# Kernel optimization log

Measured on AMD Instinct MI355X. Metric: run time of the kernel, lower is better.

The kernel has to match this reference:

```python
import jax, jax.numpy as jnp
import numpy as np

N_NODES = 100000
N_EDGES = 1000000
IN_FEATS = 128
HID_FEATS = 128
OUT_FEATS = 128
N_CLASSES = 16
NEG_SLOPE = 0.01
BN_EPS = 1e-5


def _linear_params(key, d_in, d_out):
    k1, k2 = jax.random.split(key)
    s = 1.0 / np.sqrt(d_in)
    w = jax.random.uniform(k1, (d_in, d_out), jnp.float32, -s, s)
    b = jax.random.uniform(k2, (d_out,), jnp.float32, -s, s)
    return w, b


def setup_inputs() -> dict:
    key = jax.random.key(0)
    ks = jax.random.split(key, 16)
    node_feat = jax.random.normal(ks[0], (N_NODES, IN_FEATS), jnp.float32)
    src = jax.random.randint(ks[1], (N_EDGES,), 0, N_NODES, jnp.int32)
    dst = jax.random.randint(ks[2], (N_EDGES,), 0, N_NODES, jnp.int32)
    dims = [(IN_FEATS, HID_FEATS), (HID_FEATS, HID_FEATS), (HID_FEATS, OUT_FEATS)]
    inp = {"node_feat": node_feat, "src": src, "dst": dst}
    for i, (din, dout) in enumerate(dims):
        wp, bp = _linear_params(ks[3 + 4 * i], din, din)      # fc_pool: d_in -> d_in
        ws, _ = _linear_params(ks[4 + 4 * i], din, dout)       # fc_self (no bias)
        wn, _ = _linear_params(ks[5 + 4 * i], din, dout)       # fc_neigh (no bias)
        _, b = _linear_params(ks[6 + 4 * i], din, dout)        # shared output bias
        inp[f"wp{i}"] = wp; inp[f"bp{i}"] = bp
        inp[f"ws{i}"] = ws; inp[f"wn{i}"] = wn; inp[f"b{i}"] = b
    inp["bn_gamma"] = jnp.ones((HID_FEATS,), jnp.float32)
    inp["bn_beta"] = jnp.zeros((HID_FEATS,), jnp.float32)
    wc, bc = _linear_params(ks[15], OUT_FEATS, N_CLASSES)
    inp["wc"] = wc; inp["bc"] = bc
    return inp


def _sage_pool(h, src, dst, deg_mask, wp, bp, ws, wn, b):
    # fc_pool + relu on source nodes, gather per edge, segment-max to dst
    hp = jax.nn.relu(h @ wp + bp)                 # [N, d_in]
    msg = hp[src]                                 # [E, d_in]
    agg = jax.ops.segment_max(msg, dst, num_segments=N_NODES)  # [N, d_in]
    agg = jnp.where(deg_mask, agg, 0.0)           # zero for isolated nodes
    return h @ ws + agg @ wn + b


def _batchnorm(x, gamma, beta):
    mu = jnp.mean(x, axis=0)
    var = jnp.var(x, axis=0)
    return (x - mu) * jax.lax.rsqrt(var + BN_EPS) * gamma + beta


def reference(node_feat, src, dst,
              wp0, bp0, ws0, wn0, b0,
              wp1, bp1, ws1, wn1, b1,
              wp2, bp2, ws2, wn2, b2,
              bn_gamma, bn_beta, wc, bc):
    deg = jnp.zeros((N_NODES,), jnp.float32).at[dst].add(1.0)
    deg_mask = (deg > 0)[:, None]
    h = jax.nn.leaky_relu(_sage_pool(node_feat, src, dst, deg_mask, wp0, bp0, ws0, wn0, b0), NEG_SLOPE)
    h = jax.nn.leaky_relu(_batchnorm(_sage_pool(h, src, dst, deg_mask, wp1, bp1, ws1, wn1, b1), bn_gamma, bn_beta), NEG_SLOPE)
    h = _sage_pool(h, src, dst, deg_mask, wp2, bp2, ws2, wn2, b2)
    return h @ wc + bc
```

## Files before the change

kernel.cpp:

```cpp
#include <hip/hip_runtime.h>


#define N_NODES 100000
#define N_EDGES 1000000
#define F 128
#define NEG_SLOPE 0.01f
#define BN_EPS 1e-5f
#define NODES_PER_XCD 12500

typedef __attribute__((ext_vector_type(8))) short bf16x8;
typedef __attribute__((ext_vector_type(4))) float f32x4;
typedef __attribute__((ext_vector_type(2))) unsigned short u16x2;

typedef __attribute__((address_space(3))) unsigned int as3_uint;
typedef __attribute__((address_space(1))) const unsigned int as1_cuint;

__device__ __forceinline__ void gload16(const void* g, void* l) {
    __builtin_amdgcn_global_load_lds((as1_cuint*)g, (as3_uint*)l, 16, 0, 0);
}

__device__ __forceinline__ unsigned short f2bf(float f) {
    unsigned int u = __float_as_uint(f);
    u += 0x7fff + ((u >> 16) & 1);
    return (unsigned short)(u >> 16);
}
__device__ __forceinline__ float bf2f(unsigned short h) {
    return __uint_as_float(((unsigned int)h) << 16);
}

__global__ __launch_bounds__(256) void zero_kernel(float4* __restrict__ p, long n4) {
    long i = (long)blockIdx.x * 256 + threadIdx.x;
    if (i < n4) p[i] = make_float4(0.f, 0.f, 0.f, 0.f);
}

__global__ __launch_bounds__(256) void f32_to_bf16_kernel(
    const float4* __restrict__ in, uint2* __restrict__ out, long n4)
{
    long i = (long)blockIdx.x * 256 + threadIdx.x;
    if (i >= n4) return;
    float4 v = in[i];
    uint2 o;
    o.x = (unsigned)f2bf(v.x) | ((unsigned)f2bf(v.y) << 16);
    o.y = (unsigned)f2bf(v.z) | ((unsigned)f2bf(v.w) << 16);
    out[i] = o;
}

__global__ __launch_bounds__(256) void pack_weights3(
    const float* __restrict__ wp, const float* __restrict__ wss,
    const float* __restrict__ wn, short* __restrict__ wp_p, short* __restrict__ wsn_p)
{
    const int i = blockIdx.x * 256 + threadIdx.x;
    if (i >= 3 * 16384) return;
    const int mat = i >> 14;
    const int idx = i & 16383;
    const int k = idx >> 7, n = idx & 127;
    const float* srcm = mat == 0 ? wp : (mat == 1 ? wss : wn);
    const int slot = ((k >> 3) * 128 + n) * 8 + (k & 7);
    if (mat == 0) wp_p[slot] = (short)f2bf(srcm[idx]);
    else wsn_p[(mat == 2 ? 16 * 128 * 8 : 0) + slot] = (short)f2bf(srcm[idx]);
}

template<int NKS>
__global__ __launch_bounds__(256) void gemm_mfma(
    const short* __restrict__ A1, const short* __restrict__ A2,
    const short* __restrict__ Bp, const float* __restrict__ bias,
    unsigned short* __restrict__ Cout, int n_rows, int act)
{
    constexpr int S = NKS / 2;
    __shared__ short tile[2 * 8192];

    const int tid = threadIdx.x;
    const int wave = tid >> 6;
    const int lane = tid & 63;
    const int m = lane & 15, q = lane >> 4;
    const int r0 = blockIdx.x * 128;
    const int rw = (wave >> 1) * 64;
    const int r0q = r0 + rw;
    const int c0 = (wave & 1) * 64;
    const int gchunk = (tid & 7) ^ ((tid >> 3) & 7);

    f32x4 acc[4][4];
#pragma unroll
    for (int i = 0; i < 4; ++i)
#pragma unroll
        for (int j = 0; j < 4; ++j)
#pragma unroll
            for (int r = 0; r < 4; ++r) acc[i][j][r] = 0.f;

    auto stage = [&](int s, int buf) {
        const short* Ap = (NKS == 8 && s >= 2) ? A2 : A1;
        const int kbase = (s & 1) * 64;
#pragma unroll
        for (int p = 0; p < 4; ++p) {
            int row = r0 + (tid >> 3) + 32 * p;
            row = min(row, n_rows - 1);
            gload16(Ap + (size_t)row * F + kbase + gchunk * 8,
                    &tile[buf * 8192 + p * 2048 + tid * 8]);
        }
    };

    stage(0, 0);
    __syncthreads();

    for (int s = 0; s < S; ++s) {
        if (s + 1 < S) stage(s + 1, (s + 1) & 1);
        const short* tb = &tile[(s & 1) * 8192];
#pragma unroll
        for (int ks2 = 0; ks2 < 2; ++ks2) {
            const int ks32 = s * 2 + ks2;
            bf16x8 b[4], a[4];
#pragma unroll
            for (int ni = 0; ni < 4; ++ni)
                b[ni] = *(const bf16x8*)(Bp + ((size_t)(ks32 * 4 + q) * F + c0 + ni * 16 + m) * 8);
#pragma unroll
            for (int mi = 0; mi < 4; ++mi)
                a[mi] = *(const bf16x8*)(tb + (rw + mi * 16 + m) * 64 + (((ks2 * 4 + q) ^ (m & 7)) << 3));
#pragma unroll
            for (int mi = 0; mi < 4; ++mi)
#pragma unroll
                for (int ni = 0; ni < 4; ++ni)
                    acc[mi][ni] = __builtin_amdgcn_mfma_f32_16x16x32_bf16(a[mi], b[ni], acc[mi][ni], 0, 0, 0);
        }
        __syncthreads();
    }

    float bv[4];
#pragma unroll
    for (int ni = 0; ni < 4; ++ni) bv[ni] = bias[c0 + ni * 16 + m];

    short* ep = &tile[wave * 1280];
    const int colc_lo = m >> 3, cin = m & 7;
#pragma unroll
    for (int mi = 0; mi < 4; ++mi) {
#pragma unroll
        for (int ni = 0; ni < 4; ++ni) {
            const int colc = 2 * ni + colc_lo;
#pragma unroll
            for (int rg = 0; rg < 4; ++rg) {
                const int row16 = q * 4 + rg;
                float v = acc[mi][ni][rg] + bv[ni];
                if (act == 1) v = v > 0.f ? v : 0.f;
                else if (act == 2) v = v > 0.f ? v : v * NEG_SLOPE;
                ep[row16 * 80 + ((colc ^ (row16 & 7)) << 3) + cin] = (short)f2bf(v);
            }
        }
        __syncthreads();
#pragma unroll
        for (int p = 0; p < 2; ++p) {
            const int lrow = (lane >> 3) + 8 * p;
            bf16x8 vv = *(const bf16x8*)&ep[lrow * 80 + (((lane & 7) ^ (lrow & 7)) << 3)];
            const int grow = r0q + mi * 16 + lrow;
            if (grow < n_rows)
                *(bf16x8*)(Cout + (size_t)grow * F + c0 + ((lane & 7) << 3)) = vv;
        }
        __syncthreads();
    }
}

__global__ __launch_bounds__(256) void hist_kernel(const int* __restrict__ dst, int* __restrict__ deg) {
    const int e = blockIdx.x * 256 + threadIdx.x;
    if (e < N_EDGES) atomicAdd(&deg[__builtin_nontemporal_load(&dst[e])], 1);
}

__global__ __launch_bounds__(256) void scan1_kernel(const int* __restrict__ deg, int* __restrict__ bsum) {
    __shared__ int sh[256];
    const int t = threadIdx.x;
    const int base = blockIdx.x * 1024 + t * 4;
    int s = 0;
#pragma unroll
    for (int j = 0; j < 4; ++j) s += (base + j < N_NODES) ? deg[base + j] : 0;
    sh[t] = s; __syncthreads();
    for (int off = 128; off; off >>= 1) {
        if (t < off) sh[t] += sh[t + off];
        __syncthreads();
    }
    if (t == 0) bsum[blockIdx.x] = sh[0];
}

__global__ __launch_bounds__(128) void scan2_kernel(int* __restrict__ bsum, int nb, int* __restrict__ row_start) {
    __shared__ int sh[128];
    const int t = threadIdx.x;
    sh[t] = (t < nb) ? bsum[t] : 0;
    __syncthreads();
    for (int off = 1; off < 128; off <<= 1) {
        int x = (t >= off) ? sh[t - off] : 0;
        __syncthreads();
        if (t >= off) sh[t] += x;
        __syncthreads();
    }
    if (t < nb) bsum[t] = t ? sh[t - 1] : 0;
    if (t == 0) row_start[N_NODES] = N_EDGES;
}

__global__ __launch_bounds__(256) void scan3_kernel(
    const int* __restrict__ deg, const int* __restrict__ boff,
    int* __restrict__ row_start, int* __restrict__ cursor)
{
    __shared__ int sh[256];
    const int t = threadIdx.x;
    const int base = blockIdx.x * 1024 + t * 4;
    int v[4]; int s = 0;
#pragma unroll
    for (int j = 0; j < 4; ++j) { v[j] = (base + j < N_NODES) ? deg[base + j] : 0; s += v[j]; }
    sh[t] = s; __syncthreads();
    for (int off = 1; off < 256; off <<= 1) {
        int x = (t >= off) ? sh[t - off] : 0;
        __syncthreads();
        if (t >= off) sh[t] += x;
        __syncthreads();
    }
    int excl = (t ? sh[t - 1] : 0) + boff[blockIdx.x];
#pragma unroll
    for (int j = 0; j < 4; ++j) {
        if (base + j < N_NODES) { row_start[base + j] = excl; cursor[base + j] = excl; }
        excl += v[j];
    }
}

#define CHUNK_E2 1954
__global__ __launch_bounds__(256) void scatter_xcd_kernel(
    const int* __restrict__ src, const int* __restrict__ dst,
    int* __restrict__ cursor, int* __restrict__ esrc)
{
    const int range = blockIdx.x & 7;
    const int chunk = blockIdx.x >> 3;
    const int lo = range * NODES_PER_XCD;
    const int e0 = chunk * CHUNK_E2;
    const int e1 = min(e0 + CHUNK_E2, N_EDGES);
    for (int e = e0 + threadIdx.x; e < e1; e += 256) {
        const int d = dst[e];
        if ((unsigned)(d - lo) < NODES_PER_XCD) {
            const int pos = atomicAdd(&cursor[d], 1);
            esrc[pos] = src[e];
        }
    }
}

__global__ __launch_bounds__(256) void aggregate_max_bf16(
    const unsigned int* __restrict__ hp, const int* __restrict__ row_start,
    const int* __restrict__ esrc, unsigned int* __restrict__ agg)
{
    const int node = blockIdx.x * 4 + (threadIdx.x >> 6);
    if (node >= N_NODES) return;
    const int lane = threadIdx.x & 63;
    const int beg = row_start[node], end = row_start[node + 1];
    u16x2 mm = (u16x2)0;
    for (int base = beg; base < end; base += 16) {
        int s[16];
#pragma unroll
        for (int j = 0; j < 16; ++j) {
            const int t = base + j;
            s[j] = esrc[(t < end) ? t : beg];
        }
        unsigned int v[16];
#pragma unroll
        for (int j = 0; j < 16; ++j) v[j] = hp[(size_t)s[j] * 64 + lane];
#pragma unroll
        for (int j = 0; j < 16; ++j)
            mm = __builtin_elementwise_max(mm, __builtin_bit_cast(u16x2, v[j]));
    }
    agg[(size_t)node * 64 + lane] = __builtin_bit_cast(unsigned int, mm);
}

#define BN_ROWS_PER_BLOCK 196
__global__ __launch_bounds__(256) void bn_stats_kernel(
    const unsigned short* __restrict__ x, float* __restrict__ stats, int n)
{
    const int tid = threadIdx.x;
    const int wave = tid >> 6, lane = tid & 63;
    const int rgrp = lane >> 4;
    const int c16 = lane & 15;
    const int rbase = blockIdx.x * BN_ROWS_PER_BLOCK;
    const int rend = min(rbase + BN_ROWS_PER_BLOCK, n);

    float s[8], ss[8];
#pragma unroll
    for (int j = 0; j < 8; ++j) { s[j] = 0.f; ss[j] = 0.f; }

    for (int r = rbase + wave * 4 + rgrp; r < rend; r += 16) {
        const uint4 v = *(const uint4*)(x + (size_t)r * F + c16 * 8);
        const unsigned int w[4] = {v.x, v.y, v.z, v.w};
#pragma unroll
        for (int u = 0; u < 4; ++u) {
            const float f0 = bf2f((unsigned short)(w[u] & 0xffffu));
            const float f1 = bf2f((unsigned short)(w[u] >> 16));
            s[2*u]   += f0; ss[2*u]   = fmaf(f0, f0, ss[2*u]);
            s[2*u+1] += f1; ss[2*u+1] = fmaf(f1, f1, ss[2*u+1]);
        }
    }
#pragma unroll
    for (int j = 0; j < 8; ++j) {
        s[j]  += __shfl_down(s[j], 32);  s[j]  += __shfl_down(s[j], 16);
        ss[j] += __shfl_down(ss[j], 32); ss[j] += __shfl_down(ss[j], 16);
    }
    __shared__ float sh[4][16][16];
    if (lane < 16) {
#pragma unroll
        for (int j = 0; j < 8; ++j) {
            sh[wave][c16][2*j]     = s[j];
            sh[wave][c16][2*j + 1] = ss[j];
        }
    }
    __syncthreads();
    const float tot = sh[0][tid >> 4][tid & 15] + sh[1][tid >> 4][tid & 15]
                    + sh[2][tid >> 4][tid & 15] + sh[3][tid >> 4][tid & 15];
    const int col = (tid >> 4) * 8 + ((tid >> 1) & 7);
    atomicAdd(&stats[(tid & 1) * 128 + col], tot);
}

__global__ void bn_finalize_kernel(
    const float* __restrict__ stats, const float* __restrict__ gamma,
    const float* __restrict__ beta, float* __restrict__ coef)
{
    const int c = threadIdx.x;
    const float mean = stats[c] * (1.f / N_NODES);
    const float var = stats[128 + c] * (1.f / N_NODES) - mean * mean;
    const float scale = gamma[c] * rsqrtf(var + BN_EPS);
    coef[c] = scale;
    coef[128 + c] = fmaf(-mean, scale, beta[c]);
}

__global__ __launch_bounds__(256) void bn_apply_bf16(
    unsigned int* __restrict__ x, const float* __restrict__ coef, long n2)
{
    __shared__ float sc[128], sf[128];
    if (threadIdx.x < 128) {
        sc[threadIdx.x] = coef[threadIdx.x];
        sf[threadIdx.x] = coef[128 + threadIdx.x];
    }
    __syncthreads();
    const long i = (long)blockIdx.x * 256 + threadIdx.x;
    if (i >= n2) return;
    const unsigned int v = x[i];
    const int c0 = (int)(i & 63) * 2;
    float a = fmaf(bf2f((unsigned short)(v & 0xffffu)), sc[c0], sf[c0]);
    float b = fmaf(bf2f((unsigned short)(v >> 16)), sc[c0 + 1], sf[c0 + 1]);
    a = a > 0.f ? a : a * NEG_SLOPE;
    b = b > 0.f ? b : b * NEG_SLOPE;
    x[i] = (unsigned)f2bf(a) | ((unsigned)f2bf(b) << 16);
}

__global__ __launch_bounds__(256) void classifier_kernel(
    const unsigned short* __restrict__ X, const float* __restrict__ Wc,
    const float* __restrict__ bc, float* __restrict__ out, int n)
{
    __shared__ float Wl[2048];
    __shared__ float Xs[16 * 132];
    const int tid = threadIdx.x;
    for (int i = tid; i < 2048; i += 256) Wl[i] = Wc[i];
    const int r0 = blockIdx.x * 16;
    for (int i = tid; i < 2048; i += 256) {
        const int row = i >> 7, col = i & 127;
        const int gr = r0 + row;
        Xs[row * 132 + col] = (gr < n) ? bf2f(X[(size_t)gr * F + col]) : 0.f;
    }
    __syncthreads();
    const int rl = tid >> 4, c = tid & 15;
    const int r = r0 + rl;
    if (r >= n) return;
    float s = bc[c];
    const float* xr = &Xs[rl * 132];
#pragma unroll
    for (int k = 0; k < 128; ++k) s = fmaf(xr[k], Wl[k * 16 + c], s);
    out[(size_t)r * 16 + c] = s;
}

extern "C" void kernel_launch(void* const* d_in, const int* in_sizes, int n_in,
                              void* d_out, int out_size, void* d_ws, size_t ws_size,
                              hipStream_t stream) {
    const float* node_feat = (const float*)d_in[0];
    const int* src = (const int*)d_in[1];
    const int* dst = (const int*)d_in[2];
    const float* wp[3] = {(const float*)d_in[3],  (const float*)d_in[8],  (const float*)d_in[13]};
    const float* bp[3] = {(const float*)d_in[4],  (const float*)d_in[9],  (const float*)d_in[14]};
    const float* wsm[3] = {(const float*)d_in[5], (const float*)d_in[10], (const float*)d_in[15]};
    const float* wn[3] = {(const float*)d_in[6],  (const float*)d_in[11], (const float*)d_in[16]};
    const float* bb[3] = {(const float*)d_in[7],  (const float*)d_in[12], (const float*)d_in[17]};
    const float* gamma = (const float*)d_in[18];
    const float* beta  = (const float*)d_in[19];
    const float* wc    = (const float*)d_in[20];
    const float* bc    = (const float*)d_in[21];

    const size_t SZ = (size_t)N_NODES * F;
    short* sbase = (short*)d_ws;
    short* B0  = sbase;
    short* B1  = sbase + SZ;
    short* B2  = sbase + 2 * SZ;
    short* Xbf = sbase + 3 * SZ;
    short* wp_p  = sbase + 4 * SZ;
    short* wsn_p = wp_p + 3 * 16384;
    float* fbase = (float*)(wsn_p + 3 * 32768);
    float* stats = fbase;
    float* coef  = fbase + 256;
    int* ibase = (int*)(fbase + 512);
    int* deg       = ibase;
    int* row_start = ibase + 100000;
    int* cursor    = ibase + 200104;
    int* esrc      = ibase + 300104;
    int* bsum      = ibase + 1300104;

    const int gGemm = (N_NODES + 127) / 128;
    const int gE    = (N_EDGES + 255) / 256;
    const int gScan = (N_NODES + 1023) / 1024;
    const int gAgg  = (N_NODES + 3) / 4;
    const long cvt4 = (long)(SZ / 4);
    const long n2   = (long)(SZ / 2);

    f32_to_bf16_kernel<<<(int)((cvt4 + 255) / 256), 256, 0, stream>>>(
        (const float4*)node_feat, (uint2*)Xbf, cvt4);
    for (int l = 0; l < 3; ++l)
        pack_weights3<<<192, 256, 0, stream>>>(wp[l], wsm[l], wn[l],
                                               wp_p + l * 16384, wsn_p + l * 32768);

    zero_kernel<<<98, 256, 0, stream>>>((float4*)deg, 25000);
    hist_kernel<<<gE, 256, 0, stream>>>(dst, deg);
    scan1_kernel<<<gScan, 256, 0, stream>>>(deg, bsum);
    scan2_kernel<<<1, 128, 0, stream>>>(bsum, gScan, row_start);
    scan3_kernel<<<gScan, 256, 0, stream>>>(deg, bsum, row_start, cursor);
    scatter_xcd_kernel<<<4096, 256, 0, stream>>>(src, dst, cursor, esrc);

    const short* Xl[3]  = {Xbf, B0, B1};
    short* hpb[3]       = {B0, B1, B0};
    short* aggb[3]      = {B1, B2, B2};
    short* Yb[3]        = {B0, B1, B0};
    for (int l = 0; l < 3; ++l) {
        const short* X = Xl[l];
        gemm_mfma<4><<<gGemm, 256, 0, stream>>>(X, (const short*)nullptr,
            wp_p + l * 16384, bp[l], (unsigned short*)hpb[l], N_NODES, 1);
        aggregate_max_bf16<<<gAgg, 256, 0, stream>>>(
            (const unsigned int*)hpb[l], row_start, esrc, (unsigned int*)aggb[l]);
        const int act = (l == 0) ? 2 : 0;
        gemm_mfma<8><<<gGemm, 256, 0, stream>>>(X, aggb[l],
            wsn_p + l * 32768, bb[l], (unsigned short*)Yb[l], N_NODES, act);
        if (l == 1) {
            zero_kernel<<<1, 256, 0, stream>>>((float4*)stats, 64);
            bn_stats_kernel<<<512, 256, 0, stream>>>(
                (const unsigned short*)Yb[l], stats, N_NODES);
            bn_finalize_kernel<<<1, 128, 0, stream>>>(stats, gamma, beta, coef);
            bn_apply_bf16<<<(int)((n2 + 255) / 256), 256, 0, stream>>>(
                (unsigned int*)Yb[l], coef, n2);
        }
    }
    classifier_kernel<<<(N_NODES + 15) / 16, 256, 0, stream>>>(
        (const unsigned short*)B0, wc, bc, (float*)d_out, N_NODES);
}
```

Measured before the change: 554.6 us.

## Fuse prep kernels and overlap edge scatter with layer-0 pool GEMM

Three pieces of setup work are merged into one launch each. The feature conversion, degree histogram and weight packing now run as one prep kernel, and the two zeroing launches become one. The CSR edge scatter and the first fc_pool GEMM now share a single kernel with interleaved block roles, so the GEMM can fill the machine while the scatter is bound by atomics. The scatter also loads 16 edges per thread with batched atomics. This removes several launches and their gaps, at the cost of heterogeneous blocks competing for resources such as LDS and registers in the fused kernel.

Measured after the change: 529.2 us. 1.05x faster.

```diff
diff --git a/kernel.cpp b/kernel.cpp
--- a/kernel.cpp
+++ b/kernel.cpp
@@ -28,43 +28,71 @@
     return __uint_as_float(((unsigned int)h) << 16);
 }
 
-__global__ __launch_bounds__(256) void zero_kernel(float4* __restrict__ p, long n4) {
-    long i = (long)blockIdx.x * 256 + threadIdx.x;
-    if (i < n4) p[i] = make_float4(0.f, 0.f, 0.f, 0.f);
-}
-
-__global__ __launch_bounds__(256) void f32_to_bf16_kernel(
-    const float4* __restrict__ in, uint2* __restrict__ out, long n4)
-{
-    long i = (long)blockIdx.x * 256 + threadIdx.x;
-    if (i >= n4) return;
-    float4 v = in[i];
-    uint2 o;
-    o.x = (unsigned)f2bf(v.x) | ((unsigned)f2bf(v.y) << 16);
-    o.y = (unsigned)f2bf(v.z) | ((unsigned)f2bf(v.w) << 16);
-    out[i] = o;
-}
-
-__global__ __launch_bounds__(256) void pack_weights3(
-    const float* __restrict__ wp, const float* __restrict__ wss,
-    const float* __restrict__ wn, short* __restrict__ wp_p, short* __restrict__ wsn_p)
-{
-    const int i = blockIdx.x * 256 + threadIdx.x;
-    if (i >= 3 * 16384) return;
-    const int mat = i >> 14;
-    const int idx = i & 16383;
-    const int k = idx >> 7, n = idx & 127;
-    const float* srcm = mat == 0 ? wp : (mat == 1 ? wss : wn);
-    const int slot = ((k >> 3) * 128 + n) * 8 + (k & 7);
-    if (mat == 0) wp_p[slot] = (short)f2bf(srcm[idx]);
-    else wsn_p[(mat == 2 ? 16 * 128 * 8 : 0) + slot] = (short)f2bf(srcm[idx]);
+__global__ __launch_bounds__(256) void zero_misc_kernel(
+    float4* __restrict__ deg4, float4* __restrict__ stats4)
+{
+    if (blockIdx.x < 98) {
+        const int i = blockIdx.x * 256 + threadIdx.x;
+        if (i < 25000) deg4[i] = make_float4(0.f, 0.f, 0.f, 0.f);
+    } else {
+        if (threadIdx.x < 64) stats4[threadIdx.x] = make_float4(0.f, 0.f, 0.f, 0.f);
+    }
+}
+
+#define PREP_GROUPS 4483
+__global__ __launch_bounds__(256) void prep_kernel(
+    const float4* __restrict__ nf, uint2* __restrict__ xout,
+    const int* __restrict__ dst, int* __restrict__ deg,
+    const float* __restrict__ w0, const float* __restrict__ w1, const float* __restrict__ w2,
+    const float* __restrict__ w3, const float* __restrict__ w4, const float* __restrict__ w5,
+    const float* __restrict__ w6, const float* __restrict__ w7, const float* __restrict__ w8,
+    short* __restrict__ wp_p, short* __restrict__ wsn_p)
+{
+    const int g = blockIdx.x >> 2;
+    const int k = blockIdx.x & 3;
+    const int tid = threadIdx.x;
+    if (k < 3) {
+        const int c = g * 3 + k;
+        if (c >= 12500) return;
+        const long i = (long)c * 256 + tid;
+        float4 v = nf[i];
+        uint2 o;
+        o.x = (unsigned)f2bf(v.x) | ((unsigned)f2bf(v.y) << 16);
+        o.y = (unsigned)f2bf(v.z) | ((unsigned)f2bf(v.w) << 16);
+        xout[i] = o;
+        return;
+    }
+    if (g < 3907) {
+        const int e = g * 256 + tid;
+        if (e < N_EDGES) atomicAdd(&deg[__builtin_nontemporal_load(&dst[e])], 1);
+        return;
+    }
+    const int po = g - 3907;
+    if (po >= 576) return;
+    const int idx = po * 256 + tid;
+    const int matid = idx >> 14;
+    const int layer = (matid * 11) >> 5;
+    const int mat = matid - 3 * layer;
+    const int i = idx & 16383;
+    const int kk = i >> 7, n = i & 127;
+    const float* srcm;
+    switch (matid) {
+        case 0: srcm = w0; break; case 1: srcm = w1; break; case 2: srcm = w2; break;
+        case 3: srcm = w3; break; case 4: srcm = w4; break; case 5: srcm = w5; break;
+        case 6: srcm = w6; break; case 7: srcm = w7; break; default: srcm = w8; break;
+    }
+    const int slot = ((kk >> 3) * 128 + n) * 8 + (kk & 7);
+    const short v = (short)f2bf(srcm[i]);
+    if (mat == 0) wp_p[layer * 16384 + slot] = v;
+    else wsn_p[layer * 32768 + (mat == 2 ? 16384 : 0) + slot] = v;
 }
 
 template<int NKS>
-__global__ __launch_bounds__(256) void gemm_mfma(
+__device__ __forceinline__ void gemm_body(
+    const int bid,
     const short* __restrict__ A1, const short* __restrict__ A2,
     const short* __restrict__ Bp, const float* __restrict__ bias,
-    unsigned short* __restrict__ Cout, int n_rows, int act)
+    unsigned short* __restrict__ Cout, const int n_rows, const int act)
 {
     constexpr int S = NKS / 2;
     __shared__ short tile[2 * 8192];
@@ -73,7 +101,7 @@
     const int wave = tid >> 6;
     const int lane = tid & 63;
     const int m = lane & 15, q = lane >> 4;
-    const int r0 = blockIdx.x * 128;
+    const int r0 = bid * 128;
     const int rw = (wave >> 1) * 64;
     const int r0q = r0 + rw;
     const int c0 = (wave & 1) * 64;
@@ -157,9 +185,13 @@
     }
 }
 
-__global__ __launch_bounds__(256) void hist_kernel(const int* __restrict__ dst, int* __restrict__ deg) {
-    const int e = blockIdx.x * 256 + threadIdx.x;
-    if (e < N_EDGES) atomicAdd(&deg[__builtin_nontemporal_load(&dst[e])], 1);
+template<int NKS>
+__global__ __launch_bounds__(256) void gemm_mfma(
+    const short* __restrict__ A1, const short* __restrict__ A2,
+    const short* __restrict__ Bp, const float* __restrict__ bias,
+    unsigned short* __restrict__ Cout, int n_rows, int act)
+{
+    gemm_body<NKS>(blockIdx.x, A1, A2, Bp, bias, Cout, n_rows, act);
 }
 
 __global__ __launch_bounds__(256) void scan1_kernel(const int* __restrict__ deg, int* __restrict__ bsum) {
@@ -217,22 +249,45 @@
     }
 }
 
-#define CHUNK_E2 1954
-__global__ __launch_bounds__(256) void scatter_xcd_kernel(
+__global__ __launch_bounds__(256) void scatter_gemm_kernel(
     const int* __restrict__ src, const int* __restrict__ dst,
-    int* __restrict__ cursor, int* __restrict__ esrc)
-{
-    const int range = blockIdx.x & 7;
-    const int chunk = blockIdx.x >> 3;
-    const int lo = range * NODES_PER_XCD;
-    const int e0 = chunk * CHUNK_E2;
-    const int e1 = min(e0 + CHUNK_E2, N_EDGES);
-    for (int e = e0 + threadIdx.x; e < e1; e += 256) {
-        const int d = dst[e];
-        if ((unsigned)(d - lo) < NODES_PER_XCD) {
-            const int pos = atomicAdd(&cursor[d], 1);
-            esrc[pos] = src[e];
-        }
+    int* __restrict__ cursor, int* __restrict__ esrc,
+    const short* __restrict__ A1, const short* __restrict__ Bp,
+    const float* __restrict__ bias, unsigned short* __restrict__ Cout)
+{
+    const int bid = blockIdx.x;
+    const int grp = bid >> 3;
+    const int t8 = bid & 7;
+    const int sgrp = grp / 7;
+    const int u = grp - sgrp * 7;
+    if (u < 5) {
+        const int lo = t8 * NODES_PER_XCD;
+        const int chunk = sgrp * 5 + u;
+        const int e0 = chunk * 4096 + threadIdx.x;
+        int d[16]; bool hit[16];
+#pragma unroll
+        for (int j = 0; j < 16; ++j) {
+            const int e = e0 + j * 256;
+            d[j] = dst[min(e, N_EDGES - 1)];
+        }
+#pragma unroll
+        for (int j = 0; j < 16; ++j)
+            hit[j] = (e0 + j * 256 < N_EDGES) & ((unsigned)(d[j] - lo) < (unsigned)NODES_PER_XCD);
+        int sv[16];
+#pragma unroll
+        for (int j = 0; j < 16; ++j)
+            if (hit[j]) sv[j] = src[e0 + j * 256];
+        int pos[16];
+#pragma unroll
+        for (int j = 0; j < 16; ++j)
+            if (hit[j]) pos[j] = atomicAdd(&cursor[d[j]], 1);
+#pragma unroll
+        for (int j = 0; j < 16; ++j)
+            if (hit[j]) esrc[pos[j]] = sv[j];
+    } else {
+        const int g = (sgrp * 2 + (u - 5)) * 8 + t8;
+        if (g >= (N_NODES + 127) / 128) return;
+        gemm_body<4>(g, A1, (const short*)nullptr, Bp, bias, Cout, N_NODES, 1);
     }
 }
 
@@ -400,24 +455,24 @@
     int* bsum      = ibase + 1300104;
 
     const int gGemm = (N_NODES + 127) / 128;
-    const int gE    = (N_EDGES + 255) / 256;
     const int gScan = (N_NODES + 1023) / 1024;
     const int gAgg  = (N_NODES + 3) / 4;
-    const long cvt4 = (long)(SZ / 4);
     const long n2   = (long)(SZ / 2);
 
-    f32_to_bf16_kernel<<<(int)((cvt4 + 255) / 256), 256, 0, stream>>>(
-        (const float4*)node_feat, (uint2*)Xbf, cvt4);
-    for (int l = 0; l < 3; ++l)
-        pack_weights3<<<192, 256, 0, stream>>>(wp[l], wsm[l], wn[l],
-                                               wp_p + l * 16384, wsn_p + l * 32768);
-
-    zero_kernel<<<98, 256, 0, stream>>>((float4*)deg, 25000);
-    hist_kernel<<<gE, 256, 0, stream>>>(dst, deg);
+    zero_misc_kernel<<<99, 256, 0, stream>>>((float4*)deg, (float4*)stats);
+
+    prep_kernel<<<PREP_GROUPS * 4, 256, 0, stream>>>(
+        (const float4*)node_feat, (uint2*)Xbf, dst, deg,
+        wp[0], wsm[0], wn[0], wp[1], wsm[1], wn[1], wp[2], wsm[2], wn[2],
+        wp_p, wsn_p);
+
     scan1_kernel<<<gScan, 256, 0, stream>>>(deg, bsum);
     scan2_kernel<<<1, 128, 0, stream>>>(bsum, gScan, row_start);
     scan3_kernel<<<gScan, 256, 0, stream>>>(deg, bsum, row_start, cursor);
-    scatter_xcd_kernel<<<4096, 256, 0, stream>>>(src, dst, cursor, esrc);
+
+    scatter_gemm_kernel<<<2744, 256, 0, stream>>>(
+        src, dst, cursor, esrc,
+        Xbf, wp_p, bp[0], (unsigned short*)B0);
 
     const short* Xl[3]  = {Xbf, B0, B1};
     short* hpb[3]       = {B0, B1, B0};
@@ -425,15 +480,15 @@
     short* Yb[3]        = {B0, B1, B0};
     for (int l = 0; l < 3; ++l) {
         const short* X = Xl[l];
-        gemm_mfma<4><<<gGemm, 256, 0, stream>>>(X, (const short*)nullptr,
-            wp_p + l * 16384, bp[l], (unsigned short*)hpb[l], N_NODES, 1);
+        if (l > 0)
+            gemm_mfma<4><<<gGemm, 256, 0, stream>>>(X, (const short*)nullptr,
+                wp_p + l * 16384, bp[l], (unsigned short*)hpb[l], N_NODES, 1);
         aggregate_max_bf16<<<gAgg, 256, 0, stream>>>(
             (const unsigned int*)hpb[l], row_start, esrc, (unsigned int*)aggb[l]);
         const int act = (l == 0) ? 2 : 0;
         gemm_mfma<8><<<gGemm, 256, 0, stream>>>(X, aggb[l],
             wsn_p + l * 32768, bb[l], (unsigned short*)Yb[l], N_NODES, act);
         if (l == 1) {
-            zero_kernel<<<1, 256, 0, stream>>>((float4*)stats, 64);
             bn_stats_kernel<<<512, 256, 0, stream>>>(
                 (const unsigned short*)Yb[l], stats, N_NODES);
             bn_finalize_kernel<<<1, 128, 0, stream>>>(stats, gamma, beta, coef);
```
